# Optimization experiments

Hardware: AMD Instinct MI355X
Metric: run time of the kernel (lower is better)

The kernel has to match this reference:

```python
import jax, jax.numpy as jnp
import numpy as np

D_MODEL = 1024
N_HEADS = 16
HEAD_DIM = D_MODEL // N_HEADS
D_FF = 4096
LN_EPS = 1e-5


def setup_inputs() -> dict:
    key = jax.random.key(0)
    ks = jax.random.split(key, 13)
    s = lambda fan_in: 1.0 / np.sqrt(fan_in)
    return {
        "x": jax.random.normal(ks[0], (2, 2048, D_MODEL), dtype=jnp.float32),
        "w_qkv": jax.random.uniform(ks[1], (D_MODEL, 3 * D_MODEL), jnp.float32, -s(D_MODEL), s(D_MODEL)),
        "b_qkv": jax.random.uniform(ks[2], (3 * D_MODEL,), jnp.float32, -s(D_MODEL), s(D_MODEL)),
        "w_out": jax.random.uniform(ks[3], (D_MODEL, D_MODEL), jnp.float32, -s(D_MODEL), s(D_MODEL)),
        "b_out": jax.random.uniform(ks[4], (D_MODEL,), jnp.float32, -s(D_MODEL), s(D_MODEL)),
        "w_ff1": jax.random.uniform(ks[5], (D_MODEL, D_FF), jnp.float32, -s(D_MODEL), s(D_MODEL)),
        "b_ff1": jax.random.uniform(ks[6], (D_FF,), jnp.float32, -s(D_MODEL), s(D_MODEL)),
        "w_ff2": jax.random.uniform(ks[7], (D_FF, D_MODEL), jnp.float32, -s(D_FF), s(D_FF)),
        "b_ff2": jax.random.uniform(ks[8], (D_MODEL,), jnp.float32, -s(D_FF), s(D_FF)),
        "ln1_g": jnp.ones((D_MODEL,), jnp.float32),
        "ln1_b": jnp.zeros((D_MODEL,), jnp.float32),
        "ln2_g": jnp.ones((D_MODEL,), jnp.float32),
        "ln2_b": jnp.zeros((D_MODEL,), jnp.float32),
    }


def _layer_norm(x, g, b):
    mu = jnp.mean(x, axis=-1, keepdims=True)
    var = jnp.mean(jnp.square(x - mu), axis=-1, keepdims=True)
    return (x - mu) * jax.lax.rsqrt(var + LN_EPS) * g + b


def reference(x, w_qkv, b_qkv, w_out, b_out, w_ff1, b_ff1, w_ff2, b_ff2,
              ln1_g, ln1_b, ln2_g, ln2_b):
    B, S, D = x.shape
    scale = HEAD_DIM ** -0.5
    qkv = x @ w_qkv + b_qkv                                   # [B,S,3D]
    qkv = qkv.reshape(B, S, 3, N_HEADS, HEAD_DIM)
    q, k, v = (qkv[:, :, 0], qkv[:, :, 1], qkv[:, :, 2])      # [B,S,H,Dh]
    attn = jnp.einsum("bqhd,bkhd->bhqk", q, k) * scale        # [B,H,S,S]
    attn = jax.nn.softmax(attn, axis=-1)
    o = jnp.einsum("bhqk,bkhd->bqhd", attn, v).reshape(B, S, D)
    o = o @ w_out + b_out
    x = _layer_norm(x + o, ln1_g, ln1_b)
    # FFN: Linear -> exact GELU -> Linear (dropout = 0)
    h = jax.nn.gelu(x @ w_ff1 + b_ff1, approximate=False)
    ff = h @ w_ff2 + b_ff2
    x = _layer_norm(x + ff, ln2_g, ln2_b)
    return x
```

## Files before the change

### kernel.cpp

```cpp
#include <hip/hip_runtime.h>
#include <hip/hip_bf16.h>
#include <cstdint>
#include <cstddef>

using bf16 = __hip_bfloat16;
typedef __attribute__((ext_vector_type(8))) short bf16x8;
typedef __attribute__((ext_vector_type(4))) float f32x4;

#define TOKENS 4096
#define DMODEL 1024
#define DFF    4096
#define SEQ    2048
#define NHEAD  16
#define HDIM   64
#define KVBLK  64
#define NT     (SEQ / KVBLK)
#define QSCALE 0.1803368801111f

__device__ __forceinline__ void async16(const void* g, void* l) {
  __builtin_amdgcn_global_load_lds(
      (const __attribute__((address_space(1))) void*)g,
      (__attribute__((address_space(3))) void*)l, 16, 0, 0);
}

__device__ __forceinline__ f32x4 mfma16(bf16x8 a, bf16x8 b, f32x4 c) {
  return __builtin_amdgcn_mfma_f32_16x16x32_bf16(a, b, c, 0, 0, 0);
}

__device__ __forceinline__ float exp2_fast(float x) {
  float r;
  asm("v_exp_f32 %0, %1" : "=v"(r) : "v"(x));
  return r;
}

__device__ __forceinline__ float gelu_fast(float x) {
  const float z = fabsf(x) * 0.70710678118f;
  const float t = __builtin_amdgcn_rcpf(1.f + 0.3275911f * z);
  float p = 1.061405429f;
  p = p * t - 1.453152027f;
  p = p * t + 1.421413741f;
  p = p * t - 0.284496736f;
  p = p * t + 0.254829592f;
  const float e = exp2_fast(-z * z * 1.44269504089f);
  float erf = 1.f - p * t * e;
  erf = (x < 0.f) ? -erf : erf;
  return 0.5f * x * (1.f + erf);
}

__global__ void cast_bf16_k(const float* __restrict__ src, bf16* __restrict__ dst, int n) {
  int i = (blockIdx.x * blockDim.x + threadIdx.x) * 4;
  if (i >= n) return;
  float4 v = *(const float4*)(src + i);
  dst[i + 0] = __float2bfloat16(v.x);
  dst[i + 1] = __float2bfloat16(v.y);
  dst[i + 2] = __float2bfloat16(v.z);
  dst[i + 3] = __float2bfloat16(v.w);
}

__global__ void transpose_cast_k(const float* __restrict__ src, bf16* __restrict__ dst,
                                 int K, int N) {
  __shared__ float tile[32][33];
  int nt = blockIdx.x * 32, kt = blockIdx.y * 32;
  int tx = threadIdx.x, ty = threadIdx.y;
  #pragma unroll
  for (int i = 0; i < 32; i += 8)
    tile[ty + i][tx] = src[(size_t)(kt + ty + i) * N + nt + tx];
  __syncthreads();
  #pragma unroll
  for (int i = 0; i < 32; i += 8)
    dst[(size_t)(nt + ty + i) * K + kt + tx] = __float2bfloat16(tile[tx][ty + i]);
}

template <int EPI, int BN>
__global__ __launch_bounds__(256, 2)
void gemm_bt(const bf16* __restrict__ A, const bf16* __restrict__ Bt,
             const float* __restrict__ bias, int M, int N, int K,
             float* __restrict__ outf, float* __restrict__ outf2,
             bf16* __restrict__ outb,
             bf16* __restrict__ Qb, bf16* __restrict__ Kb, bf16* __restrict__ Vtb) {
  constexpr int MR = (BN == 128) ? 4 : 2;
  __shared__ bf16 Al[2][128 * 32];
  __shared__ bf16 Bl[2][BN * 32];
  const int t = threadIdx.x;
  const int nwg = gridDim.x * gridDim.y;
  const int flat = blockIdx.y * gridDim.x + blockIdx.x;
  const int swz = (flat & 7) * (nwg >> 3) + (flat >> 3);
  const int bm = (swz / gridDim.x) * 128, bn = (swz % gridDim.x) * BN;
  const int kz = blockIdx.z;
  const int Ksub = K / gridDim.z;
  const int kb0 = kz * Ksub;
  const int wid = t >> 6, lane = t & 63, g = lane >> 4, r = lane & 15;
  const int wr = (BN == 128) ? (wid >> 1) * 64 : wid * 32;
  const int wc = (BN == 128) ? (wid & 1) * 64 : 0;

  const f32x4 zero = {0.f, 0.f, 0.f, 0.f};
  f32x4 acc[MR][4];
  #pragma unroll
  for (int i = 0; i < MR; i++)
    #pragma unroll
    for (int j = 0; j < 4; j++) acc[i][j] = zero;

  const int ar0 = t >> 2, ac = (t & 3) * 8;
  const int ar1 = ar0 + 64;
  const int ach0 = t * 16, ach1 = ach0 + 4096;

  const int NK = Ksub >> 5;
  #define STAGE(ktile, pb)                                                          \
    do {                                                                            \
      const int kk = kb0 + ((ktile) << 5);                                          \
      async16(A + (size_t)(bm + ar0) * K + kk + ac, (char*)Al[pb] + ach0);          \
      async16(A + (size_t)(bm + ar1) * K + kk + ac, (char*)Al[pb] + ach1);          \
      async16(Bt + (size_t)(bn + ar0) * K + kk + ac, (char*)Bl[pb] + ach0);         \
      if constexpr (BN == 128)                                                      \
        async16(Bt + (size_t)(bn + ar1) * K + kk + ac, (char*)Bl[pb] + ach1);       \
    } while (0)

  STAGE(0, 0);
  asm volatile("s_waitcnt vmcnt(0)" ::: "memory");
  __builtin_amdgcn_s_barrier();

  #pragma unroll 1
  for (int it = 0; it < NK; ++it) {
    const int cur = it & 1;
    if (it + 1 < NK) STAGE(it + 1, cur ^ 1);
    bf16x8 af[MR], bfr[4];
    #pragma unroll
    for (int mt = 0; mt < MR; mt++)
      af[mt] = *(const bf16x8*)&Al[cur][(wr + mt * 16 + r) * 32 + 8 * g];
    #pragma unroll
    for (int nt = 0; nt < 4; nt++)
      bfr[nt] = *(const bf16x8*)&Bl[cur][(wc + nt * 16 + r) * 32 + 8 * g];
    #pragma unroll
    for (int mt = 0; mt < MR; mt++)
      #pragma unroll
      for (int nt = 0; nt < 4; nt++)
        acc[mt][nt] = mfma16(af[mt], bfr[nt], acc[mt][nt]);
    __builtin_amdgcn_sched_barrier(0);
    asm volatile("s_waitcnt vmcnt(0)" ::: "memory");
    __builtin_amdgcn_s_barrier();
  }
  #undef STAGE

  float* __restrict__ pdst = kz ? outf2 : outf;
  #pragma unroll
  for (int nt = 0; nt < 4; nt++) {
    const int col = bn + wc + nt * 16 + r;
    const float bv = (EPI == 3) ? 0.f : bias[col];
    #pragma unroll
    for (int mt = 0; mt < MR; mt++) {
      #pragma unroll
      for (int j = 0; j < 4; j++) {
        const int row = bm + wr + mt * 16 + 4 * g + j;
        float v = acc[mt][nt][j] + bv;
        if constexpr (EPI == 0) {
          const int part = col >> 10, hd = col & 1023, h = hd >> 6, d = hd & 63;
          const int b_ = row >> 11, s_ = row & 2047;
          if (part == 0) {
            Qb[((size_t)(b_ * NHEAD + h) * SEQ + s_) * HDIM + d] =
                __float2bfloat16(v * QSCALE);
          } else if (part == 1) {
            Kb[((size_t)(b_ * NHEAD + h) * SEQ + s_) * HDIM + d] = __float2bfloat16(v);
          } else {
            Vtb[((size_t)(b_ * NHEAD + h) * HDIM + d) * SEQ + s_] = __float2bfloat16(v);
          }
        } else if constexpr (EPI == 3) {
          pdst[(size_t)row * N + col] = v;
        } else {
          outb[(size_t)row * N + col] = __float2bfloat16(gelu_fast(v));
        }
      }
    }
  }
}

__global__ __launch_bounds__(256, 3)
void attn_k(const bf16* __restrict__ Q, const bf16* __restrict__ Km,
            const bf16* __restrict__ Vt, bf16* __restrict__ O) {
  __shared__ bf16 Kl[2][KVBLK * 64];
  __shared__ bf16 Vl[2][KVBLK * 64];
  __shared__ bf16 P[4][32 * 64];
  const int b = blockIdx.x;
  const int bswz = (b & 7) * 64 + (b >> 3);
  const int bh = bswz >> 4, qb = bswz & 15;
  const int t = threadIdx.x, wid = t >> 6, lane = t & 63, g = lane >> 4, r = lane & 15;
  const int q0 = qb * 128 + wid * 32;
  const bf16* Qp = Q + (size_t)bh * SEQ * HDIM;
  const char* Kc = (const char*)(Km + (size_t)bh * SEQ * HDIM);
  const char* Vc = (const char*)(Vt + (size_t)bh * HDIM * SEQ);

  bf16x8 qf[2][2];
  #pragma unroll
  for (int s = 0; s < 2; s++) {
    qf[s][0] = *(const bf16x8*)&Qp[(q0 + 16 * s + r) * HDIM + 8 * g];
    qf[s][1] = *(const bf16x8*)&Qp[(q0 + 16 * s + r) * HDIM + 8 * g + 32];
  }

  const int o0 = wid * 2048 + lane * 16, o1 = o0 + 1024;
  const int cs0 = ((((o0 >> 4) & 7) ^ ((o0 >> 7) & 7)) << 4);
  const int cs1 = ((((o1 >> 4) & 7) ^ ((o1 >> 7) & 7)) << 4);
  const int kso0 = (o0 & ~127) + cs0, kso1 = (o1 & ~127) + cs1;
  const int vso0 = (o0 >> 7) * (SEQ * 2) + cs0, vso1 = (o1 >> 7) * (SEQ * 2) + cs1;

  const f32x4 zero = {0.f, 0.f, 0.f, 0.f};
  f32x4 oacc[2][4];
  #pragma unroll
  for (int s = 0; s < 2; s++)
    #pragma unroll
    for (int i = 0; i < 4; i++) oacc[s][i] = zero;
  float mrow[2] = {-1e30f, -1e30f}, lrow[2] = {0.f, 0.f};
  bf16* pl = P[wid];
  const int cA = ((g ^ (r & 7)) << 3), cB = (((g + 4) ^ (r & 7)) << 3);

  {
    char* kd = (char*)Kl[0]; char* vd = (char*)Vl[0];
    async16(Kc + kso0, kd + o0); async16(Kc + kso1, kd + o1);
    async16(Vc + vso0, vd + o0); async16(Vc + vso1, vd + o1);
  }

  #pragma unroll 1
  for (int tt = 0; tt < NT; ++tt) {
    if (tt + 1 < NT) {
      const char* ks = Kc + (tt + 1) * (KVBLK * HDIM * 2);
      const char* vs = Vc + (tt + 1) * (KVBLK * 2);
      char* kd = (char*)Kl[(tt + 1) & 1]; char* vd = (char*)Vl[(tt + 1) & 1];
      async16(ks + kso0, kd + o0); async16(ks + kso1, kd + o1);
      async16(vs + vso0, vd + o0); async16(vs + vso1, vd + o1);
      asm volatile("s_waitcnt vmcnt(4)" ::: "memory");
    } else {
      asm volatile("s_waitcnt vmcnt(0)" ::: "memory");
    }
    __builtin_amdgcn_sched_barrier(0);
    __builtin_amdgcn_s_barrier();
    __builtin_amdgcn_sched_barrier(0);

    const bf16* kbuf = Kl[tt & 1];
    const bf16* vbuf = Vl[tt & 1];

    f32x4 sacc[2][4];
    #pragma unroll
    for (int kt = 0; kt < 4; kt++) {
      const bf16* krow = kbuf + (kt * 16 + r) * 64;
      bf16x8 ka = *(const bf16x8*)&krow[cA];
      bf16x8 kb = *(const bf16x8*)&krow[cB];
      #pragma unroll
      for (int s = 0; s < 2; s++) {
        f32x4 sc = mfma16(ka, qf[s][0], zero);
        sacc[s][kt] = mfma16(kb, qf[s][1], sc);
      }
    }

    bool grow[2];
    float corr[2];
    #pragma unroll
    for (int s = 0; s < 2; s++) {
      float m0 = fmaxf(fmaxf(sacc[s][0][0], sacc[s][0][1]), fmaxf(sacc[s][0][2], sacc[s][0][3]));
      float m1 = fmaxf(fmaxf(sacc[s][1][0], sacc[s][1][1]), fmaxf(sacc[s][1][2], sacc[s][1][3]));
      float m2 = fmaxf(fmaxf(sacc[s][2][0], sacc[s][2][1]), fmaxf(sacc[s][2][2], sacc[s][2][3]));
      float m3 = fmaxf(fmaxf(sacc[s][3][0], sacc[s][3][1]), fmaxf(sacc[s][3][2], sacc[s][3][3]));
      float mx = fmaxf(fmaxf(m0, m1), fmaxf(m2, m3));
      mx = fmaxf(mx, __shfl_xor(mx, 16));
      mx = fmaxf(mx, __shfl_xor(mx, 32));
      grow[s] = !__all(mx <= mrow[s] + 8.f);
      corr[s] = 1.f;
      if (grow[s]) {
        const float mn = fmaxf(mrow[s], mx);
        corr[s] = exp2_fast(mrow[s] - mn);
        mrow[s] = mn;
      }
      float sum = 0.f;
      #pragma unroll
      for (int kt = 0; kt < 4; kt++) {
        bf16 pk[4];
        #pragma unroll
        for (int j = 0; j < 4; j++) {
          const float p = exp2_fast(sacc[s][kt][j] - mrow[s]);
          pk[j] = __float2bfloat16(p);
          sum += p;
        }
        const int pc = (((kt * 2 + (g >> 1)) ^ (r & 7)) << 4) + ((g & 1) << 3);
        *(short4*)((char*)pl + (16 * s + r) * 128 + pc) = *(const short4*)pk;
      }
      sum += __shfl_xor(sum, 16);
      sum += __shfl_xor(sum, 32);
      lrow[s] = lrow[s] * corr[s] + sum;
    }

    asm volatile("s_waitcnt lgkmcnt(0)" ::: "memory");
    __builtin_amdgcn_sched_barrier(0);
    bf16x8 pf[2][2];
    #pragma unroll
    for (int s = 0; s < 2; s++) {
      pf[s][0] = *(const bf16x8*)((const char*)pl + (16 * s + r) * 128 + (cA << 1));
      pf[s][1] = *(const bf16x8*)((const char*)pl + (16 * s + r) * 128 + (cB << 1));
    }

    #pragma unroll
    for (int s = 0; s < 2; s++) {
      if (grow[s]) {
        float cq[4];
        #pragma unroll
        for (int j = 0; j < 4; j++) cq[j] = __shfl(corr[s], 4 * g + j);
        #pragma unroll
        for (int dt = 0; dt < 4; dt++)
          #pragma unroll
          for (int j = 0; j < 4; j++) oacc[s][dt][j] *= cq[j];
      }
    }

    #pragma unroll
    for (int dt = 0; dt < 4; dt++) {
      const bf16* vrow = vbuf + (dt * 16 + r) * 64;
      bf16x8 v0 = *(const bf16x8*)&vrow[cA];
      bf16x8 v1 = *(const bf16x8*)&vrow[cB];
      #pragma unroll
      for (int s = 0; s < 2; s++) {
        oacc[s][dt] = mfma16(pf[s][0], v0, oacc[s][dt]);
        oacc[s][dt] = mfma16(pf[s][1], v1, oacc[s][dt]);
      }
    }
    __builtin_amdgcn_sched_barrier(0);
    __builtin_amdgcn_s_barrier();
  }

  const int b_ = bh >> 4, h = bh & 15;
  #pragma unroll
  for (int s = 0; s < 2; s++) {
    float lq[4];
    #pragma unroll
    for (int j = 0; j < 4; j++) lq[j] = __shfl(lrow[s], 4 * g + j);
    #pragma unroll
    for (int dt = 0; dt < 4; dt++)
      #pragma unroll
      for (int j = 0; j < 4; j++) {
        const int tok = b_ * SEQ + q0 + 16 * s + 4 * g + j;
        O[(size_t)tok * DMODEL + h * HDIM + dt * 16 + r] =
            __float2bfloat16(oacc[s][dt][j] / lq[j]);
      }
  }
}

__global__ __launch_bounds__(256)
void ln_fused_k(const float* __restrict__ p0, const float* __restrict__ p1,
                const float* __restrict__ bias2, const float* __restrict__ resid,
                const float* __restrict__ gw, const float* __restrict__ bw,
                float* __restrict__ outf, bf16* __restrict__ outb) {
  const int row = blockIdx.x, t = threadIdx.x;
  const size_t base = (size_t)row * DMODEL + t * 4;
  const float4 a = *(const float4*)(p0 + base);
  const float4 b = *(const float4*)(p1 + base);
  const float4 rr = *(const float4*)(resid + base);
  const float4 bb = *(const float4*)(bias2 + t * 4);
  float4 v;
  v.x = a.x + b.x + rr.x + bb.x;
  v.y = a.y + b.y + rr.y + bb.y;
  v.z = a.z + b.z + rr.z + bb.z;
  v.w = a.w + b.w + rr.w + bb.w;
  float s = v.x + v.y + v.z + v.w;
  float s2 = v.x * v.x + v.y * v.y + v.z * v.z + v.w * v.w;
  #pragma unroll
  for (int m = 1; m < 64; m <<= 1) { s += __shfl_xor(s, m); s2 += __shfl_xor(s2, m); }
  __shared__ float red[8];
  const int wid = t >> 6, lane = t & 63;
  if (lane == 0) { red[wid] = s; red[4 + wid] = s2; }
  __syncthreads();
  s = red[0] + red[1] + red[2] + red[3];
  s2 = red[4] + red[5] + red[6] + red[7];
  const float mu = s * (1.f / DMODEL);
  const float rstd = rsqrtf(s2 * (1.f / DMODEL) - mu * mu + 1e-5f);
  const float4 gv = *(const float4*)(gw + t * 4);
  const float4 bv = *(const float4*)(bw + t * 4);
  float o0 = (v.x - mu) * rstd * gv.x + bv.x;
  float o1 = (v.y - mu) * rstd * gv.y + bv.y;
  float o2 = (v.z - mu) * rstd * gv.z + bv.z;
  float o3 = (v.w - mu) * rstd * gv.w + bv.w;
  if (outf) {
    float4 ov = {o0, o1, o2, o3};
    *(float4*)(outf + base) = ov;
  }
  if (outb) {
    bf16* p = outb + base;
    p[0] = __float2bfloat16(o0); p[1] = __float2bfloat16(o1);
    p[2] = __float2bfloat16(o2); p[3] = __float2bfloat16(o3);
  }
}

extern "C" void kernel_launch(void* const* d_in, const int* in_sizes, int n_in,
                              void* d_out, int out_size, void* d_ws, size_t ws_size,
                              hipStream_t stream) {
  const float* x     = (const float*)d_in[0];
  const float* w_qkv = (const float*)d_in[1];
  const float* b_qkv = (const float*)d_in[2];
  const float* w_out = (const float*)d_in[3];
  const float* b_out = (const float*)d_in[4];
  const float* w_ff1 = (const float*)d_in[5];
  const float* b_ff1 = (const float*)d_in[6];
  const float* w_ff2 = (const float*)d_in[7];
  const float* b_ff2 = (const float*)d_in[8];
  const float* ln1_g = (const float*)d_in[9];
  const float* ln1_b = (const float*)d_in[10];
  const float* ln2_g = (const float*)d_in[11];
  const float* ln2_b = (const float*)d_in[12];
  float* out = (float*)d_out;

  char* base = (char*)d_ws;
  bf16* wqkvT = (bf16*)(base);
  bf16* woutT = (bf16*)(base + 6291456);
  bf16* wff1T = (bf16*)(base + 8388608);
  bf16* wff2T = (bf16*)(base + 16777216);
  bf16* Qb    = (bf16*)(base + 25165824);
  bf16* Kb    = (bf16*)(base + 33554432);
  bf16* Vtb   = (bf16*)(base + 41943040);
  bf16* xob   = (bf16*)(base + 50331648);
  bf16* hb    = (bf16*)(base + 25165824);
  float* pA0  = (float*)(base + 25165824);
  float* pA1  = (float*)(base + 58720256);
  float* pB0  = (float*)(base + 58720256);
  float* pB1  = (float*)(base);
  float* x1f  = (float*)(base + 75497472);
  bf16* x1b   = (bf16*)(base + 92274688);
  (void)in_sizes; (void)n_in; (void)out_size; (void)ws_size;

  dim3 tb(32, 8);
  transpose_cast_k<<<dim3(3072 / 32, 1024 / 32), tb, 0, stream>>>(w_qkv, wqkvT, 1024, 3072);
  transpose_cast_k<<<dim3(1024 / 32, 1024 / 32), tb, 0, stream>>>(w_out, woutT, 1024, 1024);
  transpose_cast_k<<<dim3(4096 / 32, 1024 / 32), tb, 0, stream>>>(w_ff1, wff1T, 1024, 4096);
  transpose_cast_k<<<dim3(1024 / 32, 4096 / 32), tb, 0, stream>>>(w_ff2, wff2T, 4096, 1024);
  cast_bf16_k<<<(TOKENS * DMODEL / 4 + 255) / 256, 256, 0, stream>>>(x, xob, TOKENS * DMODEL);

  gemm_bt<0, 128><<<dim3(3072 / 128, TOKENS / 128), 256, 0, stream>>>(
      xob, wqkvT, b_qkv, TOKENS, 3072, 1024, nullptr, nullptr, nullptr, Qb, Kb, Vtb);
  attn_k<<<dim3(512), 256, 0, stream>>>(Qb, Kb, Vtb, xob);
  gemm_bt<3, 64><<<dim3(1024 / 64, TOKENS / 128, 2), 256, 0, stream>>>(
      xob, woutT, b_out, TOKENS, 1024, 1024, pA0, pA1, nullptr, nullptr, nullptr, nullptr);
  ln_fused_k<<<TOKENS, 256, 0, stream>>>(pA0, pA1, b_out, x, ln1_g, ln1_b, x1f, x1b);
  gemm_bt<2, 128><<<dim3(4096 / 128, TOKENS / 128), 256, 0, stream>>>(
      x1b, wff1T, b_ff1, TOKENS, 4096, 1024, nullptr, nullptr, hb, nullptr, nullptr, nullptr);
  gemm_bt<3, 64><<<dim3(1024 / 64, TOKENS / 128, 2), 256, 0, stream>>>(
      hb, wff2T, b_ff2, TOKENS, 1024, 4096, pB0, pB1, nullptr, nullptr, nullptr, nullptr);
  ln_fused_k<<<TOKENS, 256, 0, stream>>>(pB0, pB1, b_ff2, x1f, ln2_g, ln2_b, out, nullptr);
}
```

Baseline: 267.0 us.

## Split attention KV range across two blocks and merge partials in a combine kernel

Each attention block now processes only half of the key/value sequence, doubling the grid to increase CU occupancy. Unnormalized fp32 partial outputs plus per-row max and sum are written to workspace. A new combine kernel rescales and merges the two halves and writes bf16 output in token layout. This adds extra global traffic for fp32 partials and an extra kernel launch.

```diff
diff --git a/kernel.cpp b/kernel.cpp
--- a/kernel.cpp
+++ b/kernel.cpp
@@ -175,18 +175,22 @@
 
 __global__ __launch_bounds__(256, 3)
 void attn_k(const bf16* __restrict__ Q, const bf16* __restrict__ Km,
-            const bf16* __restrict__ Vt, bf16* __restrict__ O) {
+            const bf16* __restrict__ Vt, float* __restrict__ Opart,
+            float* __restrict__ ML) {
   __shared__ bf16 Kl[2][KVBLK * 64];
   __shared__ bf16 Vl[2][KVBLK * 64];
   __shared__ bf16 P[4][32 * 64];
   const int b = blockIdx.x;
-  const int bswz = (b & 7) * 64 + (b >> 3);
-  const int bh = bswz >> 4, qb = bswz & 15;
+  const int bswz = (b & 7) * 128 + (b >> 3);
+  const int bh = bswz >> 5, sub = bswz & 31;
+  const int half = sub >> 4, qb = sub & 15;
   const int t = threadIdx.x, wid = t >> 6, lane = t & 63, g = lane >> 4, r = lane & 15;
   const int q0 = qb * 128 + wid * 32;
   const bf16* Qp = Q + (size_t)bh * SEQ * HDIM;
-  const char* Kc = (const char*)(Km + (size_t)bh * SEQ * HDIM);
-  const char* Vc = (const char*)(Vt + (size_t)bh * HDIM * SEQ);
+  const char* Kc = (const char*)(Km + (size_t)bh * SEQ * HDIM) +
+                   (size_t)half * (SEQ / 2) * HDIM * 2;
+  const char* Vc = (const char*)(Vt + (size_t)bh * HDIM * SEQ) +
+                   (size_t)half * (SEQ / 2) * 2;
 
   bf16x8 qf[2][2];
   #pragma unroll
@@ -217,9 +221,10 @@
     async16(Vc + vso0, vd + o0); async16(Vc + vso1, vd + o1);
   }
 
+  const int NT2 = NT / 2;
   #pragma unroll 1
-  for (int tt = 0; tt < NT; ++tt) {
-    if (tt + 1 < NT) {
+  for (int tt = 0; tt < NT2; ++tt) {
+    if (tt + 1 < NT2) {
       const char* ks = Kc + (tt + 1) * (KVBLK * HDIM * 2);
       const char* vs = Vc + (tt + 1) * (KVBLK * 2);
       char* kd = (char*)Kl[(tt + 1) & 1]; char* vd = (char*)Vl[(tt + 1) & 1];
@@ -322,21 +327,44 @@
     __builtin_amdgcn_s_barrier();
   }
 
-  const int b_ = bh >> 4, h = bh & 15;
+  float* Oq = Opart + (size_t)(half * 32 + bh) * SEQ * HDIM;
   #pragma unroll
   for (int s = 0; s < 2; s++) {
-    float lq[4];
-    #pragma unroll
-    for (int j = 0; j < 4; j++) lq[j] = __shfl(lrow[s], 4 * g + j);
     #pragma unroll
     for (int dt = 0; dt < 4; dt++)
       #pragma unroll
       for (int j = 0; j < 4; j++) {
-        const int tok = b_ * SEQ + q0 + 16 * s + 4 * g + j;
-        O[(size_t)tok * DMODEL + h * HDIM + dt * 16 + r] =
-            __float2bfloat16(oacc[s][dt][j] / lq[j]);
-      }
-  }
+        const int row = q0 + 16 * s + 4 * g + j;
+        Oq[(size_t)row * HDIM + dt * 16 + r] = oacc[s][dt][j];
+      }
+    if (lane < 16) {
+      const size_t mi = (size_t)(half * 32 + bh) * SEQ + q0 + 16 * s + r;
+      ML[mi * 2] = mrow[s];
+      ML[mi * 2 + 1] = lrow[s];
+    }
+  }
+}
+
+__global__ __launch_bounds__(256)
+void combine_k(const float* __restrict__ Op, const float* __restrict__ ML,
+               bf16* __restrict__ O) {
+  const int gid = blockIdx.x * 256 + threadIdx.x;
+  const int row = gid >> 4;
+  const int dq = (gid & 15) << 2;
+  const float m0 = ML[(size_t)row * 2],           l0 = ML[(size_t)row * 2 + 1];
+  const float m1 = ML[(size_t)(65536 + row) * 2], l1 = ML[(size_t)(65536 + row) * 2 + 1];
+  const float M = fmaxf(m0, m1);
+  const float c0 = exp2_fast(m0 - M), c1 = exp2_fast(m1 - M);
+  const float rden = 1.f / (c0 * l0 + c1 * l1);
+  const float4 p0 = *(const float4*)&Op[(size_t)row * 64 + dq];
+  const float4 p1 = *(const float4*)&Op[(size_t)(65536 + row) * 64 + dq];
+  const int bh = row >> 11, q = row & 2047;
+  const int tok = (bh >> 4) * SEQ + q, col = (bh & 15) * 64 + dq;
+  bf16* dst = O + (size_t)tok * DMODEL + col;
+  dst[0] = __float2bfloat16((c0 * p0.x + c1 * p1.x) * rden);
+  dst[1] = __float2bfloat16((c0 * p0.y + c1 * p1.y) * rden);
+  dst[2] = __float2bfloat16((c0 * p0.z + c1 * p1.z) * rden);
+  dst[3] = __float2bfloat16((c0 * p0.w + c1 * p1.w) * rden);
 }
 
 __global__ __launch_bounds__(256)
@@ -412,6 +440,8 @@
   bf16* Vtb   = (bf16*)(base + 41943040);
   bf16* xob   = (bf16*)(base + 50331648);
   bf16* hb    = (bf16*)(base + 25165824);
+  float* Opart= (float*)(base + 58720256);
+  float* ML   = (float*)(base + 92274688);
   float* pA0  = (float*)(base + 25165824);
   float* pA1  = (float*)(base + 58720256);
   float* pB0  = (float*)(base + 58720256);
@@ -429,7 +459,8 @@
 
   gemm_bt<0, 128><<<dim3(3072 / 128, TOKENS / 128), 256, 0, stream>>>(
       xob, wqkvT, b_qkv, TOKENS, 3072, 1024, nullptr, nullptr, nullptr, Qb, Kb, Vtb);
-  attn_k<<<dim3(512), 256, 0, stream>>>(Qb, Kb, Vtb, xob);
+  attn_k<<<dim3(1024), 256, 0, stream>>>(Qb, Kb, Vtb, Opart, ML);
+  combine_k<<<dim3(4096), 256, 0, stream>>>(Opart, ML, xob);
   gemm_bt<3, 64><<<dim3(1024 / 64, TOKENS / 128, 2), 256, 0, stream>>>(
       xob, woutT, b_out, TOKENS, 1024, 1024, pA0, pA1, nullptr, nullptr, nullptr, nullptr);
   ln_fused_k<<<TOKENS, 256, 0, stream>>>(pA0, pA1, b_out, x, ln1_g, ln1_b, x1f, x1b);
```

Result: slower. 274.5 us (+2.8%).
